# Optimization experiments

Hardware: AMD Instinct MI355X
Metric: run time of the kernel (lower is better)

The kernel has to match this reference:

```python
import jax, jax.numpy as jnp
import numpy as np

B, L, C_IN = 32, 244, 128
F_NUM, KS = 64, 5
HID = 512
SA_DIV = 3
F3 = F_NUM * 3
D_SA = F3 // SA_DIV  # must equal F_NUM (sa_div==3) for the view in SelfAttention


def setup_inputs() -> dict:
    key = jax.random.key(0)
    ks = jax.random.split(key, 16)

    def rn(k, shape, fan_in):
        return jax.random.normal(k, shape, dtype=jnp.float32) * float(np.sqrt(2.0 / fan_in))

    return {
        "x": jax.random.normal(ks[0], (B, L, C_IN), dtype=jnp.float32),
        "conv1_w": rn(ks[1], (F_NUM, 1, KS, 1), KS),
        "conv1_b": jnp.zeros((F_NUM,), jnp.float32),
        "conv2_w": rn(ks[2], (F_NUM, F_NUM, KS, 1), F_NUM * KS),
        "conv2_b": jnp.zeros((F_NUM,), jnp.float32),
        "conv3_w": rn(ks[3], (F_NUM, F_NUM, KS, 1), F_NUM * KS),
        "conv3_b": jnp.zeros((F_NUM,), jnp.float32),
        "conv4_w": rn(ks[4], (F_NUM, F_NUM, KS, 1), F_NUM * KS),
        "conv4_b": jnp.zeros((F_NUM,), jnp.float32),
        "wq": rn(ks[5], (D_SA, F3), F3),
        "wk": rn(ks[6], (D_SA, F3), F3),
        "wv": rn(ks[7], (D_SA, F3), F3),
        "wv1": rn(ks[8], (D_SA, F3), F3),
        "gamma": jnp.full((1,), 0.1, jnp.float32),
        "gru_wih": rn(ks[9], (3 * HID, F_NUM * C_IN), F_NUM * C_IN),
        "gru_whh": rn(ks[10], (3 * HID, HID), HID),
        "gru_bih": jnp.zeros((3 * HID,), jnp.float32),
        "gru_bhh": jnp.zeros((3 * HID,), jnp.float32),
        "fc_w": rn(ks[11], (1, HID), HID),
        "fc_b": jnp.zeros((1,), jnp.float32),
    }


def _conv2d(x, w, b):
    y = jax.lax.conv_general_dilated(
        x, w, window_strides=(1, 1), padding="VALID",
        dimension_numbers=("NCHW", "OIHW", "NCHW"))
    return y + b[None, :, None, None]


def reference(x, conv1_w, conv1_b, conv2_w, conv2_b, conv3_w, conv3_b, conv4_w, conv4_b,
              wq, wk, wv, wv1, gamma, gru_wih, gru_whh, gru_bih, gru_bhh, fc_w, fc_b):
    # conv stack: (B,1,L,C) -> (B,F,L',C), time dim shrinks by 4*(KS-1)
    h = x[:, None, :, :]
    h = jax.nn.relu(_conv2d(h, conv1_w, conv1_b))
    h = jax.nn.relu(_conv2d(h, conv2_w, conv2_b))
    h = jax.nn.relu(_conv2d(h, conv3_w, conv3_b))
    h = jax.nn.relu(_conv2d(h, conv4_w, conv4_b))
    Bn, Fn, Lp, Cn = h.shape
    step = int(np.ceil(Lp / 3))
    # static slice starts; last slice is x[:, :, -3:, :] (matches torch loop)
    starts = np.minimum(np.arange(step) * 3, Lp - 3)
    idx = starts[:, None] + np.arange(3)                               # (S,3)
    xs = h[:, :, idx, :]                                               # (B,F,S,3,C)
    xs = xs.transpose(0, 2, 1, 3, 4).reshape(Bn, step, Fn * 3, Cn)     # (B,S,F3,C)
    # batched SelfAttention (1x1 conv1d == matmul over channel dim)
    f = jnp.einsum("df,bsfc->bsdc", wq, xs)
    g = jnp.einsum("df,bsfc->bsdc", wk, xs)
    v = jnp.einsum("df,bsfc->bsdc", wv, xs)
    v1 = jnp.einsum("df,bsfc->bsdc", wv1, xs)
    # torch: softmax(bmm(f^T, g), dim=1) -> softmax over first C axis
    beta = jax.nn.softmax(jnp.einsum("bsdc,bsdk->bsck", f, g), axis=-2)
    o = gamma[0] * jnp.einsum("bsdc,bsck->bsdk", v, beta) + v1         # (B,S,F,C)
    seq = o.transpose(1, 0, 2, 3).reshape(step, Bn, Fn * Cn)           # (S,B,F*C)
    # single-layer GRU (PyTorch gate order r,z,n), seq-first
    xg = jnp.einsum("sbi,gi->sbg", seq, gru_wih) + gru_bih             # (S,B,3H)

    def gru_step(hprev, xg_t):
        hg = hprev @ gru_whh.T + gru_bhh
        xr, xz, xn = jnp.split(xg_t, 3, axis=-1)
        hr, hz, hn = jnp.split(hg, 3, axis=-1)
        r = jax.nn.sigmoid(xr + hr)
        z = jax.nn.sigmoid(xz + hz)
        n = jnp.tanh(xn + r * hn)
        hnew = (1.0 - z) * n + z * hprev
        return hnew, hnew

    h0 = jnp.zeros((Bn, HID), seq.dtype)
    _, outs = jax.lax.scan(gru_step, h0, xg)                            # (S,B,H)
    # temporal attention pooling over the time axis (axis 0)
    att = jnp.einsum("sbh,h->sb", outs, fc_w[0]) + fc_b[0]
    w_att = jax.nn.softmax(att, axis=0)[:, :, None]
    return jnp.sum(w_att * outs, axis=0)                                # (B,H)
```

## Files before the change

### kernel.cpp

```cpp
#include <hip/hip_runtime.h>
#include <math.h>


typedef __attribute__((ext_vector_type(8))) short short8;
typedef __attribute__((ext_vector_type(4))) float f32x4;

#define XG_STRIDE 3735552ull

__device__ inline float sigm(float x){ return 1.f/(1.f+__expf(-x)); }
__device__ inline unsigned short f2bf(float f){
    unsigned int u = __float_as_uint(f);
    u = (u + 0x7FFFu + ((u >> 16) & 1u)) >> 16;
    return (unsigned short)u;
}
__device__ inline float bf2f(unsigned short h){
    return __uint_as_float(((unsigned int)h) << 16);
}
__device__ inline int xcd_chunked(int orig, int nwg){
    int q = nwg >> 3, r = nwg & 7;
    int xcd = orig & 7, i = orig >> 3;
    return (xcd < r ? xcd*(q+1) : r*(q+1) + (xcd-r)*q) + i;
}

__global__ __launch_bounds__(256) void conv1_k(const float* __restrict__ x,
        unsigned short* __restrict__ out_h, unsigned short* __restrict__ out_l,
        const float* __restrict__ w1, const float* __restrict__ b1, int b_base)
{
    __shared__ float w1s[320];
    __shared__ float b1s[64];
    int t = threadIdx.x;
    for (int idx = t; idx < 320; idx += 256) w1s[idx] = w1[idx];
    if (t < 64)  b1s[t] = b1[t];
    __syncthreads();
    int i = blockIdx.x*256 + t;
    int c = i & 127; int t2 = i >> 7;
    int l = t2 % 240; int b = t2 / 240;
    const float* xp = x + ((size_t)(b_base + b)*244 + l)*128 + c;
    float xv[5];
    #pragma unroll
    for (int k=0;k<5;++k) xv[k] = xp[k*128];
    unsigned short* oh = out_h + (size_t)i*64;
    unsigned short* ol = out_l + (size_t)i*64;
    #pragma unroll
    for (int f8=0; f8<8; ++f8){
        unsigned short rh[8], rl[8];
        #pragma unroll
        for (int j=0;j<8;++j){
            int f = f8*8 + j;
            float a = b1s[f];
            #pragma unroll
            for (int k=0;k<5;++k) a += w1s[f*5+k]*xv[k];
            a = a > 0.f ? a : 0.f;
            unsigned short hi = f2bf(a);
            rh[j] = hi;
            rl[j] = f2bf(a - bf2f(hi));
        }
        *(short8*)(oh + f8*8) = *(short8*)rh;
        *(short8*)(ol + f8*8) = *(short8*)rl;
    }
}

__global__ __launch_bounds__(256) void repack_convw_k(const float* __restrict__ w2,
        const float* __restrict__ w3, const float* __restrict__ w4,
        unsigned short* __restrict__ wbf_h, unsigned short* __restrict__ wbf_l)
{
    int idx = blockIdx.x*256 + threadIdx.x;
    int fi = idx & 63; int t2 = idx >> 6;
    int fo = t2 & 63;  int t3 = t2 >> 6;
    int k = t3 % 5;    int layer = t3 / 5;
    const float* ws_ = (layer==0)? w2 : (layer==1)? w3 : w4;
    float v = ws_[(fo*64 + fi)*5 + k];
    unsigned short hi = f2bf(v);
    wbf_h[idx] = hi;
    wbf_l[idx] = f2bf(v - bf2f(hi));
}

__global__ __launch_bounds__(256) void conv_mfma_s(
        const unsigned short* __restrict__ in_h, const unsigned short* __restrict__ in_l,
        unsigned short* __restrict__ out_h, unsigned short* __restrict__ out_l,
        const unsigned short* __restrict__ wk_h, const unsigned short* __restrict__ wk_l,
        const float* __restrict__ bias, int Lin, int Lout)
{
    __shared__ __align__(16) unsigned short Abh[64*72], Abl[64*72];
    __shared__ __align__(16) unsigned short Wbh[64*72], Wbl[64*72];
    int nblk = gridDim.x;
    int lin = xcd_chunked(blockIdx.x, nblk);
    int ch = lin & 1; int rest = lin >> 1;
    int l = rest % Lout; int b = rest / Lout;

    int t = threadIdx.x;
    int lane = t & 63, w = t >> 6;
    int lr = lane & 15, lh = lane >> 4;
    f32x4 acc[4];
    #pragma unroll
    for (int nf=0;nf<4;++nf) acc[nf] = (f32x4)0.f;

    const size_t ib = ((size_t)b*Lin + l)*8192 + (size_t)ch*4096;
    for (int k=0;k<5;++k){
        __syncthreads();
        #pragma unroll
        for (int i=0;i<2;++i){
            int idx = i*256 + t; int row = idx>>3, c8 = idx&7;
            *(short8*)&Abh[row*72 + c8*8] = *(const short8*)(in_h + ib + (size_t)k*8192 + idx*8);
            *(short8*)&Abl[row*72 + c8*8] = *(const short8*)(in_l + ib + (size_t)k*8192 + idx*8);
        }
        #pragma unroll
        for (int i=0;i<2;++i){
            int idx = i*256 + t; int row = idx>>3, c8 = idx&7;
            *(short8*)&Wbh[row*72 + c8*8] = *(const short8*)(wk_h + k*4096 + idx*8);
            *(short8*)&Wbl[row*72 + c8*8] = *(const short8*)(wk_l + k*4096 + idx*8);
        }
        __syncthreads();
        #pragma unroll
        for (int kk=0;kk<2;++kk){
            short8 ah, al, bh[4], blo[4];
            ah = *(const short8*)&Abh[(w*16+lr)*72 + kk*32 + lh*8];
            al = *(const short8*)&Abl[(w*16+lr)*72 + kk*32 + lh*8];
            #pragma unroll
            for (int nf=0;nf<4;++nf){
                bh[nf]  = *(const short8*)&Wbh[(nf*16+lr)*72 + kk*32 + lh*8];
                blo[nf] = *(const short8*)&Wbl[(nf*16+lr)*72 + kk*32 + lh*8];
            }
            #pragma unroll
            for (int nf=0;nf<4;++nf){
                acc[nf] = __builtin_amdgcn_mfma_f32_16x16x32_bf16(ah, bh[nf],  acc[nf], 0,0,0);
                acc[nf] = __builtin_amdgcn_mfma_f32_16x16x32_bf16(ah, blo[nf], acc[nf], 0,0,0);
                acc[nf] = __builtin_amdgcn_mfma_f32_16x16x32_bf16(al, bh[nf],  acc[nf], 0,0,0);
            }
        }
    }
    const size_t ob = ((size_t)b*Lout + l)*8192;
    #pragma unroll
    for (int nf=0;nf<4;++nf){
        int fo = nf*16 + lr;
        float bv = bias[fo];
        #pragma unroll
        for (int q=0;q<4;++q){
            int c = ch*64 + w*16 + lh*4 + q;
            float v = acc[nf][q] + bv;
            v = v > 0.f ? v : 0.f;
            unsigned short hi = f2bf(v);
            out_h[ob + c*64 + fo] = hi;
            out_l[ob + c*64 + fo] = f2bf(v - bf2f(hi));
        }
    }
}

__global__ __launch_bounds__(256) void repack_wrep_k(const float* __restrict__ wq,
        const float* __restrict__ wk, const float* __restrict__ wv,
        const float* __restrict__ wv1,
        unsigned short* __restrict__ wr_h, unsigned short* __restrict__ wr_l)
{
    int idx = blockIdx.x*256 + threadIdx.x;
    int ko = idx % 192; int md = idx / 192;
    int m = md >> 6, d = md & 63;
    int jj = ko >> 6, f = ko & 63;
    const float* src = (m==0)? wq : (m==1)? wk : (m==2)? wv : wv1;
    float v = src[d*192 + f*3 + jj];
    unsigned short hi = f2bf(v);
    wr_h[idx] = hi;
    wr_l[idx] = f2bf(v - bf2f(hi));
}

__global__ __launch_bounds__(256) void project_mfma_s(
        const unsigned short* __restrict__ h_h, const unsigned short* __restrict__ h_l,
        const unsigned short* __restrict__ wr_h, const unsigned short* __restrict__ wr_l,
        float* __restrict__ Fo, float* __restrict__ Go,
        float* __restrict__ Vo, float* __restrict__ V1o)
{
    __shared__ __align__(16) unsigned short Abh[64*72], Abl[64*72];
    __shared__ __align__(16) unsigned short Bbh[64*72], Bbl[64*72];
    int nblk = gridDim.x;
    int lin = xcd_chunked(blockIdx.x, nblk);
    int z = lin & 7; int rest = lin >> 3;
    int s = rest % 76; int bl = rest / 76;
    int mz = z >> 1, mh = z & 1;

    int t = threadIdx.x;
    int lane = t & 63, w = t >> 6;
    int wm = w >> 1, wn = w & 1;
    int lr = lane & 15, lh = lane >> 4;
    f32x4 acc[2][2];
    #pragma unroll
    for (int mf=0;mf<2;++mf)
        #pragma unroll
        for (int nf=0;nf<2;++nf) acc[mf][nf] = (f32x4)0.f;

    for (int jj=0;jj<3;++jj){
        __syncthreads();
        const size_t ao_ = ((size_t)bl*228 + 3*s + jj)*8192 + (size_t)mh*4096;
        #pragma unroll
        for (int i=0;i<2;++i){
            int idx = i*256 + t; int row = idx>>3, c8 = idx&7;
            *(short8*)&Abh[row*72 + c8*8] = *(const short8*)(h_h + ao_ + idx*8);
            *(short8*)&Abl[row*72 + c8*8] = *(const short8*)(h_l + ao_ + idx*8);
        }
        #pragma unroll
        for (int i=0;i<2;++i){
            int idx = i*256 + t; int row = idx>>3, c8 = idx&7;
            size_t wo = (size_t)(mz*64 + row)*192 + jj*64 + c8*8;
            *(short8*)&Bbh[row*72 + c8*8] = *(const short8*)(wr_h + wo);
            *(short8*)&Bbl[row*72 + c8*8] = *(const short8*)(wr_l + wo);
        }
        __syncthreads();
        #pragma unroll
        for (int kk=0;kk<2;++kk){
            short8 ah[2], al[2], bh[2], blo[2];
            #pragma unroll
            for (int mf=0;mf<2;++mf){
                ah[mf] = *(const short8*)&Abh[(wm*32+mf*16+lr)*72 + kk*32 + lh*8];
                al[mf] = *(const short8*)&Abl[(wm*32+mf*16+lr)*72 + kk*32 + lh*8];
            }
            #pragma unroll
            for (int nf=0;nf<2;++nf){
                bh[nf]  = *(const short8*)&Bbh[(wn*32+nf*16+lr)*72 + kk*32 + lh*8];
                blo[nf] = *(const short8*)&Bbl[(wn*32+nf*16+lr)*72 + kk*32 + lh*8];
            }
            #pragma unroll
            for (int mf=0;mf<2;++mf)
                #pragma unroll
                for (int nf=0;nf<2;++nf){
                    acc[mf][nf] = __builtin_amdgcn_mfma_f32_16x16x32_bf16(ah[mf], bh[nf],  acc[mf][nf], 0,0,0);
                    acc[mf][nf] = __builtin_amdgcn_mfma_f32_16x16x32_bf16(ah[mf], blo[nf], acc[mf][nf], 0,0,0);
                    acc[mf][nf] = __builtin_amdgcn_mfma_f32_16x16x32_bf16(al[mf], bh[nf],  acc[mf][nf], 0,0,0);
                }
        }
    }
    float* dst = (mz==0)? Fo : (mz==1)? Go : (mz==2)? Vo : V1o;
    size_t bs = (size_t)bl*76 + s;
    #pragma unroll
    for (int mf=0;mf<2;++mf)
        #pragma unroll
        for (int nf=0;nf<2;++nf){
            int d = wn*32 + nf*16 + lr;
            int c0 = mh*64 + wm*32 + mf*16 + lh*4;
            *(f32x4*)&dst[(bs*64 + d)*128 + c0] = acc[mf][nf];
        }
}

__global__ __launch_bounds__(256) void attend_k(const float* __restrict__ Fg,
        const float* __restrict__ Gg, const float* __restrict__ Vg,
        const float* __restrict__ V1g, const float* __restrict__ gamma,
        unsigned short* __restrict__ seq_bf, int b_base)
{
    __shared__ float sm[16384];
    int t = threadIdx.x;
    int s = blockIdx.x, bl = blockIdx.y;
    size_t base = ((size_t)bl*76 + s)*8192;
    for (int i=t; i<8192; i+=256) sm[i]      = Fg[base+i];
    for (int i=t; i<8192; i+=256) sm[8192+i] = Gg[base+i];
    __syncthreads();

    int k = t & 127, ch = t >> 7;
    float sc[64];
    #pragma unroll
    for (int j=0;j<64;++j) sc[j]=0.f;
    for (int d=0; d<64; ++d){
        float gk = sm[8192 + d*128 + k];
        #pragma unroll
        for (int cj=0; cj<16; ++cj){
            float4 f4 = *(const float4*)&sm[d*128 + ch*64 + cj*4];
            sc[cj*4+0] += f4.x*gk; sc[cj*4+1] += f4.y*gk;
            sc[cj*4+2] += f4.z*gk; sc[cj*4+3] += f4.w*gk;
        }
    }
    __syncthreads();
    float m = -1e30f;
    #pragma unroll
    for (int j=0;j<64;++j) m = fmaxf(m, sc[j]);
    sm[t] = m;
    for (int i=t; i<8192; i+=256) sm[8192+i] = Vg[base+i];
    __syncthreads();
    m = fmaxf(sm[k], sm[128+k]);
    float lsum = 0.f;
    #pragma unroll
    for (int j=0;j<64;++j){ sc[j] = __expf(sc[j]-m); lsum += sc[j]; }
    __syncthreads();
    sm[t] = lsum;
    __syncthreads();
    float rinv = 1.f/(sm[k] + sm[128+k]);
    #pragma unroll
    for (int j=0;j<64;++j) sc[j] *= rinv;
    __syncthreads();

    if (ch == 0){
        #pragma unroll
        for (int j=0;j<64;++j) sm[j*128 + k] = sc[j];
    }
    __syncthreads();

    int k2 = t & 31, dq = t >> 5;
    float ao[8][4];
    #pragma unroll
    for (int j=0;j<8;++j)
        #pragma unroll
        for (int mm=0;mm<4;++mm) ao[j][mm]=0.f;

    for (int c2=0; c2<64; ++c2){
        float bv0 = sm[c2*128 + k2],    bv1 = sm[c2*128 + k2+32];
        float bv2 = sm[c2*128 + k2+64], bv3 = sm[c2*128 + k2+96];
        #pragma unroll
        for (int j=0;j<8;++j){
            float v = sm[8192 + (dq*8+j)*128 + c2];
            ao[j][0]+=v*bv0; ao[j][1]+=v*bv1; ao[j][2]+=v*bv2; ao[j][3]+=v*bv3;
        }
    }
    __syncthreads();
    if (ch == 1){
        #pragma unroll
        for (int j=0;j<64;++j) sm[j*128 + k] = sc[j];
    }
    __syncthreads();
    for (int c2=64; c2<128; ++c2){
        float bv0 = sm[(c2-64)*128 + k2],    bv1 = sm[(c2-64)*128 + k2+32];
        float bv2 = sm[(c2-64)*128 + k2+64], bv3 = sm[(c2-64)*128 + k2+96];
        #pragma unroll
        for (int j=0;j<8;++j){
            float v = sm[8192 + (dq*8+j)*128 + c2];
            ao[j][0]+=v*bv0; ao[j][1]+=v*bv1; ao[j][2]+=v*bv2; ao[j][3]+=v*bv3;
        }
    }

    float gm = gamma[0];
    size_t sbase = (size_t)(s*32 + b_base + bl)*8192;
    #pragma unroll
    for (int j=0;j<8;++j){
        int d = dq*8+j;
        #pragma unroll
        for (int mm=0;mm<4;++mm){
            int kk = k2 + 32*mm;
            float val = gm*ao[j][mm] + V1g[base + (size_t)d*128 + kk];
            seq_bf[sbase + (size_t)d*128 + kk] = f2bf(val);
        }
    }
}

__global__ __launch_bounds__(256) void conv_wih_bf16(const float* __restrict__ w,
        unsigned short* __restrict__ o)
{
    int i = (blockIdx.x*256 + threadIdx.x)*4;
    float4 v = *(const float4*)&w[i];
    ushort4 r;
    r.x = f2bf(v.x); r.y = f2bf(v.y); r.z = f2bf(v.z); r.w = f2bf(v.w);
    *(ushort4*)&o[i] = r;
}

__global__ __launch_bounds__(512) void gemm_xg_mfma(const unsigned short* __restrict__ A,
        const unsigned short* __restrict__ Bw, const float* __restrict__ bih,
        float* __restrict__ out, int nsplit)
{
    __shared__ float AsF[128*36];
    __shared__ float BsF[128*36];
    int nwg = 228*nsplit;
    int wgid = xcd_chunked(blockIdx.x, nwg);
    int kz = wgid / 228;
    int r2 = wgid % 228;
    int n0 = (r2 % 12) * 128, m0 = (r2 / 12) * 128;
    int klen = 8192 / nsplit;
    int kbase = kz * klen;
    int nkt = klen >> 6;

    int t = threadIdx.x;
    int w = t >> 6;
    int wm = w >> 1, wn = w & 1;
    int lane = t & 63, lr = lane & 15, lh = lane >> 4;

    f32x4 acc[2][4];
    #pragma unroll
    for (int mi=0;mi<2;++mi)
        #pragma unroll
        for (int ni=0;ni<4;++ni) acc[mi][ni] = (f32x4)0.f;

    float4 ra[2], rb[2];
    #pragma unroll
    for (int i=0;i<2;++i){
        int idx = i*512 + t; int row = idx>>3, seg = idx&7;
        ra[i] = *(const float4*)(A  + (size_t)(m0 + row)*8192 + kbase + seg*8);
        rb[i] = *(const float4*)(Bw + (size_t)(n0 + row)*8192 + kbase + seg*8);
    }
    for (int kt=0; kt<nkt; ++kt){
        __syncthreads();
        #pragma unroll
        for (int i=0;i<2;++i){
            int idx = i*512 + t; int row = idx>>3, seg = idx&7;
            *(float4*)&AsF[row*36 + seg*4] = ra[i];
            *(float4*)&BsF[row*36 + seg*4] = rb[i];
        }
        __syncthreads();
        if (kt < nkt-1){
            int k0 = kbase + (kt+1)*64;
            #pragma unroll
            for (int i=0;i<2;++i){
                int idx = i*512 + t; int row = idx>>3, seg = idx&7;
                ra[i] = *(const float4*)(A  + (size_t)(m0 + row)*8192 + k0 + seg*8);
                rb[i] = *(const float4*)(Bw + (size_t)(n0 + row)*8192 + k0 + seg*8);
            }
        }
        #pragma unroll
        for (int kk=0;kk<2;++kk){
            short8 af[2], bf_[4];
            #pragma unroll
            for (int mi=0;mi<2;++mi)
                af[mi] = *(short8*)&AsF[(wm*32 + mi*16 + lr)*36 + kk*16 + lh*4];
            #pragma unroll
            for (int ni=0;ni<4;++ni)
                bf_[ni] = *(short8*)&BsF[(wn*64 + ni*16 + lr)*36 + kk*16 + lh*4];
            #pragma unroll
            for (int mi=0;mi<2;++mi)
                #pragma unroll
                for (int ni=0;ni<4;++ni)
                    acc[mi][ni] = __builtin_amdgcn_mfma_f32_16x16x32_bf16(
                                      bf_[ni], af[mi], acc[mi][ni], 0, 0, 0);
        }
    }
    float* op = out + (size_t)kz*XG_STRIDE;
    #pragma unroll
    for (int ni=0;ni<4;++ni){
        int nbase = n0 + wn*64 + ni*16 + lh*4;
        float4 bi4 = (kz == 0) ? *(const float4*)&bih[nbase]
                               : make_float4(0.f,0.f,0.f,0.f);
        #pragma unroll
        for (int mi=0;mi<2;++mi){
            int m = m0 + wm*32 + mi*16 + lr;
            float4 o;
            o.x = acc[mi][ni][0] + bi4.x;
            o.y = acc[mi][ni][1] + bi4.y;
            o.z = acc[mi][ni][2] + bi4.z;
            o.w = acc[mi][ni][3] + bi4.w;
            *(float4*)&op[(size_t)m*1536 + nbase] = o;
        }
    }
}

__global__ __launch_bounds__(256) void build_whhp_k(const float* __restrict__ whh,
        float4* __restrict__ whh_p)
{
    int idx = blockIdx.x*256 + threadIdx.x;
    int i = idx >> 9, j = idx & 511;
    float4 o;
    o.x = whh[(size_t)j*512 + i];
    o.y = whh[(size_t)(512+j)*512 + i];
    o.z = whh[(size_t)(1024+j)*512 + i];
    o.w = 0.f;
    whh_p[idx] = o;
}

__global__ __launch_bounds__(1024) void gru_lds_k(const float4* __restrict__ whh_p,
        const float* __restrict__ xg, const float* __restrict__ bhh,
        float* __restrict__ outs, float* __restrict__ hbuf,
        int* __restrict__ bar, int nsplit)
{
    __shared__ float wlr[8][516], wlz[8][516], wln[8][516];
    __shared__ float red[4][32][8][3];
    int t = threadIdx.x;
    int jc = blockIdx.x;
    int j0 = jc*8;

    #pragma unroll
    for (int it=0; it<4; ++it){
        int idx = it*1024 + t;
        int i = idx >> 3, jl = idx & 7;
        float4 w4 = whh_p[(size_t)i*512 + j0 + jl];
        wlr[jl][i] = w4.x; wlz[jl][i] = w4.y; wln[jl][i] = w4.z;
    }
    __syncthreads();

    int jl = t & 7, b = (t >> 3) & 31, iq = t >> 8;
    int volatile* cnt = bar;
    int volatile* gen = bar + 1;

    for (int s=0; s<76; ++s){
        float a0=0.f, a1=0.f, a2=0.f;
        if (s > 0){
            const float* hb = hbuf + ((s+1)&1)*16384 + b*512 + iq*128;
            const float* wr = &wlr[jl][iq*128];
            const float* wz = &wlz[jl][iq*128];
            const float* wn = &wln[jl][iq*128];
            #pragma unroll 4
            for (int i=0;i<128;++i){
                float hv = hb[i];
                a0 += wr[i]*hv; a1 += wz[i]*hv; a2 += wn[i]*hv;
            }
        }
        red[iq][b][jl][0]=a0; red[iq][b][jl][1]=a1; red[iq][b][jl][2]=a2;
        __syncthreads();
        if (t < 256){
            int jl2 = t & 7, b2 = t >> 3;
            int j2 = j0 + jl2;
            float hr=0.f, hz=0.f, hn=0.f;
            #pragma unroll
            for (int q=0;q<4;++q){
                hr += red[q][b2][jl2][0];
                hz += red[q][b2][jl2][1];
                hn += red[q][b2][jl2][2];
            }
            size_t xi = (size_t)(s*32 + b2)*1536 + j2;
            float xr = xg[xi], xz = xg[xi+512], xn = xg[xi+1024];
            if (nsplit == 2){
                xr += xg[xi + XG_STRIDE];
                xz += xg[xi + 512 + XG_STRIDE];
                xn += xg[xi + 1024 + XG_STRIDE];
            }
            hr += bhh[j2]; hz += bhh[512+j2]; hn += bhh[1024+j2];
            float r = sigm(xr+hr), z = sigm(xz+hz);
            float n = tanhf(xn + r*hn);
            float hp = (s==0) ? 0.f : hbuf[((s+1)&1)*16384 + b2*512 + j2];
            float hnew = (1.f - z)*n + z*hp;
            hbuf[(s&1)*16384 + (size_t)b2*512 + j2] = hnew;
            outs[(size_t)s*16384 + (size_t)b2*512 + j2] = hnew;
        }
        __syncthreads();
        if (t == 0){
            __threadfence();
            int g = __hip_atomic_load((int*)gen, __ATOMIC_RELAXED,
                                      __HIP_MEMORY_SCOPE_AGENT);
            int arrived = __hip_atomic_fetch_add((int*)cnt, 1, __ATOMIC_ACQ_REL,
                                                 __HIP_MEMORY_SCOPE_AGENT);
            if (arrived == 63){
                __hip_atomic_store((int*)cnt, 0, __ATOMIC_RELAXED,
                                   __HIP_MEMORY_SCOPE_AGENT);
                __hip_atomic_fetch_add((int*)gen, 1, __ATOMIC_ACQ_REL,
                                       __HIP_MEMORY_SCOPE_AGENT);
            } else {
                while (__hip_atomic_load((int*)gen, __ATOMIC_ACQUIRE,
                                         __HIP_MEMORY_SCOPE_AGENT) == g)
                    __builtin_amdgcn_s_sleep(1);
            }
            __threadfence();
        }
        __syncthreads();
    }
}

__global__ __launch_bounds__(256) void pool_k(const float* __restrict__ outs,
        const float* __restrict__ fcw, const float* __restrict__ fcb,
        float* __restrict__ out)
{
    __shared__ float att[80], watt[128];
    int b = blockIdx.x, t = threadIdx.x;
    int w = t >> 6, lane = t & 63;
    for (int s = w; s < 76; s += 4){
        float acc = 0.f;
        const float* op = outs + (size_t)s*16384 + (size_t)b*512;
        #pragma unroll
        for (int hh = 0; hh < 512; hh += 64) acc += op[hh+lane]*fcw[hh+lane];
        #pragma unroll
        for (int off=32; off; off>>=1) acc += __shfl_down(acc, off);
        if (lane==0) att[s] = acc + fcb[0];
    }
    __syncthreads();
    if (t < 64){
        float a0 = (t<76)? att[t] : -1e30f;
        float a1 = (t+64<76)? att[t+64] : -1e30f;
        float m = fmaxf(a0,a1);
        #pragma unroll
        for (int off=32; off; off>>=1) m = fmaxf(m, __shfl_xor(m, off));
        float e0 = (t<76)? __expf(a0-m) : 0.f;
        float e1 = (t+64<76)? __expf(a1-m) : 0.f;
        float ssum = e0+e1;
        #pragma unroll
        for (int off=32; off; off>>=1) ssum += __shfl_xor(ssum, off);
        float ri = 1.f/ssum;
        watt[t] = e0*ri;
        watt[t+64] = e1*ri;
    }
    __syncthreads();
    for (int h = t; h < 512; h += 256){
        float acc=0.f;
        for (int s=0;s<76;++s) acc += watt[s]*outs[(size_t)s*16384 + (size_t)b*512 + h];
        out[(size_t)b*512 + h] = acc;
    }
}

extern "C" void kernel_launch(void* const* d_in, const int* in_sizes, int n_in,
                              void* d_out, int out_size, void* d_ws, size_t ws_size,
                              hipStream_t stream)
{
    const float* x   = (const float*)d_in[0];
    const float* w1  = (const float*)d_in[1];  const float* b1  = (const float*)d_in[2];
    const float* w2  = (const float*)d_in[3];  const float* b2  = (const float*)d_in[4];
    const float* w3  = (const float*)d_in[5];  const float* b3  = (const float*)d_in[6];
    const float* w4  = (const float*)d_in[7];  const float* b4  = (const float*)d_in[8];
    const float* wq  = (const float*)d_in[9];  const float* wk  = (const float*)d_in[10];
    const float* wv  = (const float*)d_in[11]; const float* wv1 = (const float*)d_in[12];
    const float* gamma = (const float*)d_in[13];
    const float* wih = (const float*)d_in[14]; const float* whh = (const float*)d_in[15];
    const float* bih = (const float*)d_in[16]; const float* bhh = (const float*)d_in[17];
    const float* fcw = (const float*)d_in[18]; const float* fcb = (const float*)d_in[19];

    int nb = 2, ns = 1;
    {
        auto need = [](int nb_, int ns_)->size_t{
            return ((size_t)nb_*4521984ull + 16117760ull
                    + (size_t)(ns_-1)*3735552ull + 40000ull)*4ull + 4096ull;
        };
        if      (ws_size >= need(8,2)){ nb = 8; ns = 2; }
        else if (ws_size >= need(4,2)){ nb = 4; ns = 2; }
        else if (ws_size >= need(2,2)){ nb = 2; ns = 2; }
    }

    float* ws = (float*)d_ws;
    size_t off = 0;
    size_t szAh = (size_t)nb*983040ull;
    size_t szBh = (size_t)nb*966656ull;
    size_t szP  = (size_t)nb*622592ull;
    unsigned short* bufAh = (unsigned short*)(ws + off); off += szAh;
    unsigned short* bufAl = (unsigned short*)(ws + off); off += szAh;
    unsigned short* bufBh = (unsigned short*)(ws + off); off += szBh;
    unsigned short* bufBl = (unsigned short*)(ws + off); off += szBh;
    float* V1b = ws + off; off += szP;
    unsigned short* seq_bf = (unsigned short*)(ws + off); off += 9961472ull;
    float* xg   = ws + off; off += (size_t)ns*XG_STRIDE;
    float* outs = ws + off; off += 77ull*16384;
    float4* whh_p = (float4*)(ws + off); off += 1048576ull;
    float* hbuf = ws + off; off += 32768ull;
    int* bar = (int*)(ws + off); off += 16ull;
    unsigned short* wbf_h = (unsigned short*)(ws + off); off += 30720ull;
    unsigned short* wbf_l = (unsigned short*)(ws + off); off += 30720ull;
    unsigned short* wr_h  = (unsigned short*)(ws + off); off += 24576ull;
    unsigned short* wr_l  = (unsigned short*)(ws + off); off += 24576ull;

    float* Fb = (float*)bufAh;
    float* Gb = Fb + szP;
    float* Vb = Fb + 2*szP;
    unsigned short* wih_bf = bufAh;

    hipMemsetAsync(bar, 0, 8, stream);
    repack_convw_k<<<240, 256, 0, stream>>>(w2, w3, w4, wbf_h, wbf_l);
    repack_wrep_k<<<192, 256, 0, stream>>>(wq, wk, wv, wv1, wr_h, wr_l);
    build_whhp_k<<<1024, 256, 0, stream>>>(whh, whh_p);

    int nchunks = 32 / nb;
    for (int chunk=0; chunk<nchunks; ++chunk){
        int b_base = chunk*nb;
        conv1_k<<<nb*120, 256, 0, stream>>>(x, bufAh, bufAl, w1, b1, b_base);
        conv_mfma_s<<<236*nb*2, 256, 0, stream>>>(bufAh, bufAl, bufBh, bufBl,
                                                  wbf_h, wbf_l, b2, 240, 236);
        conv_mfma_s<<<232*nb*2, 256, 0, stream>>>(bufBh, bufBl, bufAh, bufAl,
                                                  wbf_h+20480, wbf_l+20480, b3, 236, 232);
        conv_mfma_s<<<228*nb*2, 256, 0, stream>>>(bufAh, bufAl, bufBh, bufBl,
                                                  wbf_h+40960, wbf_l+40960, b4, 232, 228);
        project_mfma_s<<<76*nb*8, 256, 0, stream>>>(bufBh, bufBl, wr_h, wr_l,
                                                    Fb, Gb, Vb, V1b);
        attend_k<<<dim3(76,nb), 256, 0, stream>>>(Fb, Gb, Vb, V1b, gamma, seq_bf, b_base);
    }
    conv_wih_bf16<<<12288, 256, 0, stream>>>(wih, wih_bf);
    gemm_xg_mfma<<<228*ns, 512, 0, stream>>>(seq_bf, wih_bf, bih, xg, ns);
    {
        void* gargs[] = { (void*)&whh_p, (void*)&xg, (void*)&bhh,
                          (void*)&outs, (void*)&hbuf, (void*)&bar, (void*)&ns };
        hipLaunchCooperativeKernel(reinterpret_cast<void*>(gru_lds_k),
                                   dim3(64), dim3(1024), gargs, 0, stream);
    }
    pool_k<<<32, 256, 0, stream>>>(outs, fcw, fcb, (float*)d_out);
}
```

Before: 2.674 ms.

## Register-tile GRU recurrent matvec over four batches with float4 loads

Reassigns work in the GRU recurrence kernel so each thread covers a 32-element slice of the hidden input for four batch rows, instead of a 128-element slice for one batch row. Each LDS weight float4 is reused across four batches, and hidden-state reads become float4 vector loads. The cross-thread reduction grows from 4 to 16 partial sums per output, which costs more LDS space and more serial adds in the gate phase.

```diff
diff --git a/kernel.cpp b/kernel.cpp
--- a/kernel.cpp
+++ b/kernel.cpp
@@ -451,7 +451,7 @@
         int* __restrict__ bar, int nsplit)
 {
     __shared__ float wlr[8][516], wlz[8][516], wln[8][516];
-    __shared__ float red[4][32][8][3];
+    __shared__ float red[16][8][32][3];
     int t = threadIdx.x;
     int jc = blockIdx.x;
     int j0 = jc*8;
@@ -465,34 +465,49 @@
     }
     __syncthreads();
 
-    int jl = t & 7, b = (t >> 3) & 31, iq = t >> 8;
+    int jl = t & 7, iq = (t >> 3) & 15, bq = t >> 7;
+    int i0 = iq*32;
     int volatile* cnt = bar;
     int volatile* gen = bar + 1;
 
     for (int s=0; s<76; ++s){
-        float a0=0.f, a1=0.f, a2=0.f;
+        float a[4][3];
+        #pragma unroll
+        for (int bb=0;bb<4;++bb){ a[bb][0]=0.f; a[bb][1]=0.f; a[bb][2]=0.f; }
         if (s > 0){
-            const float* hb = hbuf + ((s+1)&1)*16384 + b*512 + iq*128;
-            const float* wr = &wlr[jl][iq*128];
-            const float* wz = &wlz[jl][iq*128];
-            const float* wn = &wln[jl][iq*128];
-            #pragma unroll 4
-            for (int i=0;i<128;++i){
-                float hv = hb[i];
-                a0 += wr[i]*hv; a1 += wz[i]*hv; a2 += wn[i]*hv;
-            }
-        }
-        red[iq][b][jl][0]=a0; red[iq][b][jl][1]=a1; red[iq][b][jl][2]=a2;
+            const float* hb = hbuf + ((s+1)&1)*16384;
+            #pragma unroll
+            for (int ii=0; ii<32; ii+=4){
+                int i = i0 + ii;
+                float4 wr = *(const float4*)&wlr[jl][i];
+                float4 wz = *(const float4*)&wlz[jl][i];
+                float4 wn = *(const float4*)&wln[jl][i];
+                #pragma unroll
+                for (int bb=0;bb<4;++bb){
+                    float4 h4 = *(const float4*)&hb[(bq*4+bb)*512 + i];
+                    a[bb][0] += wr.x*h4.x; a[bb][1] += wz.x*h4.x; a[bb][2] += wn.x*h4.x;
+                    a[bb][0] += wr.y*h4.y; a[bb][1] += wz.y*h4.y; a[bb][2] += wn.y*h4.y;
+                    a[bb][0] += wr.z*h4.z; a[bb][1] += wz.z*h4.z; a[bb][2] += wn.z*h4.z;
+                    a[bb][0] += wr.w*h4.w; a[bb][1] += wz.w*h4.w; a[bb][2] += wn.w*h4.w;
+                }
+            }
+        }
+        #pragma unroll
+        for (int bb=0;bb<4;++bb){
+            red[iq][jl][bq*4+bb][0] = a[bb][0];
+            red[iq][jl][bq*4+bb][1] = a[bb][1];
+            red[iq][jl][bq*4+bb][2] = a[bb][2];
+        }
         __syncthreads();
         if (t < 256){
             int jl2 = t & 7, b2 = t >> 3;
             int j2 = j0 + jl2;
             float hr=0.f, hz=0.f, hn=0.f;
             #pragma unroll
-            for (int q=0;q<4;++q){
-                hr += red[q][b2][jl2][0];
-                hz += red[q][b2][jl2][1];
-                hn += red[q][b2][jl2][2];
+            for (int q=0;q<16;++q){
+                hr += red[q][jl2][b2][0];
+                hz += red[q][jl2][b2][1];
+                hn += red[q][jl2][b2][2];
             }
             size_t xi = (size_t)(s*32 + b2)*1536 + j2;
             float xr = xg[xi], xz = xg[xi+512], xn = xg[xi+1024];
```

After: 2.884 ms. 1.08x slower.
